# Kernel tuning notes

Hardware: AMD Instinct MI355X
Metric: run time of the kernel (lower is better)

## Reference

```python
import jax, jax.numpy as jnp
import numpy as np

EPS = 1e-05


def setup_inputs() -> dict:
    key = jax.random.key(0)
    ks = jax.random.split(key, 5)
    B, Q, M, DIM = 2, 1024, 1024, 3
    H, V, OUT, C = 8, 64, 512, 8
    # Chebyshev rational coefficients of exp(-x) (first C terms), expanded per head
    cheb_coeffs_expmx = np.array([
        0.4275836, -0.546424, 0.07106222, 0.05473271,
        0.005744192, -0.00792641, -0.005392865, -0.001210823,
    ], dtype=np.float32)
    cheb_coeffs = jnp.broadcast_to(jnp.asarray(cheb_coeffs_expmx)[None, :], (H, C))
    lengthscales = jnp.asarray([0.5, 1.0, 2.0, 4.0, 8.0, 16.0, 32.0, 64.0], dtype=jnp.float32)
    return {
        "query_positions": jax.random.normal(ks[0], (B, Q, DIM), dtype=jnp.float32),
        "key_positions": jax.random.normal(ks[1], (B, M, DIM), dtype=jnp.float32),
        "values": jax.random.normal(ks[2], (B, M, H, V), dtype=jnp.float32),
        "masked_elements": jnp.zeros((B, M), dtype=bool),
        "lengthscales": lengthscales,
        "cheb_coeffs": cheb_coeffs,
        "out_w": jax.random.normal(ks[3], (OUT, H * V), dtype=jnp.float32) * (1.0 / np.sqrt(H * V)),
    }


def _cheb_scores(x, coeffs):
    # x: [B,H,Q,M] squared scaled distances; coeffs: [H,C]
    # Chebyshev rational expansion: T0=1, T1=r, Tn = 2 r T_{n-1} - T_{n-2},
    # with r = (x-1)/(x+1). Accumulate sum_c coeffs[h,c] * T_c directly
    # instead of materializing the [B,H,C,Q,M] stack (same math).
    C = coeffs.shape[1]
    r = (x - 1.0) / (x + 1.0)
    tprev = jnp.ones_like(x)
    out = coeffs[None, :, 0, None, None] * tprev
    if C >= 2:
        tcur = r
        out = out + coeffs[None, :, 1, None, None] * tcur
        for c in range(2, C):
            tnext = 2.0 * r * tcur - tprev
            out = out + coeffs[None, :, c, None, None] * tnext
            tcur, tprev = tnext, tcur
    return out


def reference(query_positions, key_positions, values, masked_elements,
              lengthscales, cheb_coeffs, out_w):
    B, Q, _ = query_positions.shape
    H = lengthscales.shape[0]
    # force_asymptotic_zero: subtract per-head mean of coefficients
    coeffs = cheb_coeffs - jnp.mean(cheb_coeffs, axis=1, keepdims=True)
    # squared pairwise distances [B,Q,M] (cdist then squared == d2)
    d2 = jnp.sum((query_positions[:, :, None, :] - key_positions[:, None, :, :]) ** 2, axis=-1)
    # scaled squared distances per head: (d/ls)^2 -> [B,H,Q,M]
    x = d2[:, None, :, :] / (lengthscales[None, :, None, None] ** 2)
    scores = _cheb_scores(x, coeffs)
    # mask memory elements, then L1-normalise over memory axis
    scores = jnp.where(masked_elements[:, None, None, :], 0.0, scores)
    scores = scores / (jnp.sum(jnp.abs(scores), axis=-1, keepdims=True) + EPS)
    # attend: [B,H,Q,M] @ [B,H,M,V] -> [B,H,Q,V]
    attended = jnp.einsum('bhqm,bmhv->bhqv', scores, values)
    # flatten heads: [B,Q,H*V], then out projection (no bias)
    flat = attended.transpose(0, 2, 1, 3).reshape(B, Q, -1)
    return flat @ out_w.T
```

## Files before the change

### kernel.cpp

```cpp
#include <hip/hip_runtime.h>
#include <hip/hip_bf16.h>


typedef __attribute__((ext_vector_type(8))) short short8v;
typedef __attribute__((ext_vector_type(4))) short short4v;
typedef __attribute__((ext_vector_type(4))) float f32x4;

#define EPSF 1e-5f

__device__ __forceinline__ float frcp(float x) { return __builtin_amdgcn_rcpf(x); }
__device__ __forceinline__ short f2bf(float f) {
    __hip_bfloat16 h = __float2bfloat16(f);
    return *reinterpret_cast<short*>(&h);
}

#define VT_ELEMS   (2u * 8u * 64u * 1024u)
#define WB_OFF_S   (VT_ELEMS)
#define FLAT_OFF_S (VT_ELEMS + 512u * 512u)

__global__ __launch_bounds__(256) void prep(
    const float* __restrict__ vals, const float* __restrict__ outw,
    short* __restrict__ vt, short* __restrict__ wb)
{
    const int bid = blockIdx.x, t = threadIdx.x;
    if (bid < 256) {
        __shared__ float sf[64 * 68];
        const int b = bid >> 7, h = (bid >> 4) & 7, m0 = (bid & 15) * 64;
        #pragma unroll
        for (int fi = 0; fi < 4; ++fi) {
            const int idx = fi * 256 + t, mr = idx >> 4, c4 = idx & 15;
            const float4 v4 = *(const float4*)&vals[
                (((size_t)b * 1024 + m0 + mr) * 8 + h) * 64 + c4 * 4];
            *(float4*)&sf[mr * 68 + c4 * 4] = v4;
        }
        __syncthreads();
        const int v = t >> 2, mo = t & 3;
        short8v o0, o1;
        #pragma unroll
        for (int i = 0; i < 8; ++i) o0[i] = f2bf(sf[(mo * 16 + i) * 68 + v]);
        #pragma unroll
        for (int i = 0; i < 8; ++i) o1[i] = f2bf(sf[(mo * 16 + 8 + i) * 68 + v]);
        const size_t ob = ((size_t)(b * 8 + h) * 64 + v) * 1024 + m0 + mo * 16;
        *(short8v*)&vt[ob] = o0;
        *(short8v*)&vt[ob + 8] = o1;
    } else {
        const int wi = bid - 256;
        #pragma unroll
        for (int k = 0; k < 8; ++k) {
            const int fidx = wi * 8192 + k * 1024 + t * 4;
            const float4 f4 = *(const float4*)&outw[fidx];
            short4v s; s[0] = f2bf(f4.x); s[1] = f2bf(f4.y);
                       s[2] = f2bf(f4.z); s[3] = f2bf(f4.w);
            *(short4v*)&wb[fidx] = s;
        }
    }
}

__global__ __launch_bounds__(512, 4) void cheb_attn(
    const float* __restrict__ qp, const float* __restrict__ kp,
    const unsigned char* __restrict__ msk,
    const float* __restrict__ ls, const float* __restrict__ cheb,
    const short* __restrict__ vt, short* __restrict__ flatb)
{
    __shared__ float s_kx[1024], s_ky[1024], s_kz[1024];
    __shared__ __align__(8) unsigned char s_mask[1024];
    __shared__ float s_l1[4][32];
    __shared__ float s_pb[3][32 * 68];

    const int t = threadIdx.x;
    const int qt = blockIdx.x, h = blockIdx.y, b = blockIdx.z;
    const int w = t >> 6, lane = t & 63;
    const int wg = w & 1, g = w >> 1;
    const int arow = lane & 15, koct = lane >> 4;

    #pragma unroll
    for (int mm_ = 0; mm_ < 2; ++mm_) {
        const int m = mm_ * 512 + t;
        const size_t base = ((size_t)b * 1024 + m) * 3;
        s_kx[m] = kp[base + 0];
        s_ky[m] = kp[base + 1];
        s_kz[m] = kp[base + 2];
    }
    *(unsigned short*)&s_mask[t * 2] =
        *(const unsigned short*)&msk[(size_t)b * 1024 + t * 2];

    const float lsv = ls[h];
    const float invls2 = 1.0f / (lsv * lsv);
    float cc[8]; float cs = 0.f;
    #pragma unroll
    for (int j = 0; j < 8; ++j) { cc[j] = cheb[h * 8 + j]; cs += cc[j]; }
    const float cm = cs * 0.125f;
    #pragma unroll
    for (int j = 0; j < 8; ++j) cc[j] -= cm;

    const int qg = qt * 32 + wg * 16 + arow;
    const float qx = qp[((size_t)b * 1024 + qg) * 3 + 0];
    const float qy = qp[((size_t)b * 1024 + qg) * 3 + 1];
    const float qz = qp[((size_t)b * 1024 + qg) * 3 + 2];

    f32x4 acc[4] = {(f32x4)(0.f), (f32x4)(0.f), (f32x4)(0.f), (f32x4)(0.f)};
    const short* vtb = vt + ((size_t)(b * 8 + h) * 64) * 1024;
    float l1p = 0.f;

    __syncthreads();

    #pragma unroll
    for (int tile = 0; tile < 4; ++tile) {
        const int m0 = g * 256 + tile * 64;

        short8v bfr[2][4];
        #pragma unroll
        for (int kk = 0; kk < 2; ++kk)
            #pragma unroll
            for (int f = 0; f < 4; ++f)
                bfr[kk][f] = *(const short8v*)
                    &vtb[(size_t)(f * 16 + arow) * 1024 + m0 + kk * 32 + koct * 8];

        f32x4 kx[2][2], ky[2][2], kz[2][2];
        uint2 mmv[2];
        #pragma unroll
        for (int kk = 0; kk < 2; ++kk) {
            const int mb = m0 + kk * 32 + koct * 8;
            kx[kk][0] = *(const f32x4*)&s_kx[mb]; kx[kk][1] = *(const f32x4*)&s_kx[mb + 4];
            ky[kk][0] = *(const f32x4*)&s_ky[mb]; ky[kk][1] = *(const f32x4*)&s_ky[mb + 4];
            kz[kk][0] = *(const f32x4*)&s_kz[mb]; kz[kk][1] = *(const f32x4*)&s_kz[mb + 4];
            mmv[kk] = *(const uint2*)&s_mask[mb];
        }

        short8v a[2];
        #pragma unroll
        for (int kk = 0; kk < 2; ++kk) {
            const bool anymask = (mmv[kk].x | mmv[kk].y) != 0u;
            #pragma unroll
            for (int j = 0; j < 8; ++j) {
                const float dx = qx - kx[kk][j >> 2][j & 3];
                const float dy = qy - ky[kk][j >> 2][j & 3];
                const float dz = qz - kz[kk][j >> 2][j & 3];
                const float x  = (dx * dx + dy * dy + dz * dz) * invls2;
                const float r  = (x - 1.f) * frcp(x + 1.f);
                const float r2 = r + r;
                float tp = 1.f, tc = r;
                float s  = cc[0] + cc[1] * r;
                #pragma unroll
                for (int c = 2; c < 8; ++c) {
                    const float tn = r2 * tc - tp;
                    s += cc[c] * tn; tp = tc; tc = tn;
                }
                if (anymask) {
                    const unsigned int mword = (j < 4) ? mmv[kk].x : mmv[kk].y;
                    if ((mword >> ((j & 3) * 8)) & 0xffu) s = 0.f;
                }
                l1p += fabsf(s);
                a[kk][j] = f2bf(s);
            }
        }

        #pragma unroll
        for (int kk = 0; kk < 2; ++kk)
            #pragma unroll
            for (int f = 0; f < 4; ++f)
                acc[f] = __builtin_amdgcn_mfma_f32_16x16x32_bf16(
                    a[kk], bfr[kk][f], acc[f], 0, 0, 0);
    }

    l1p += __shfl_xor(l1p, 16);
    l1p += __shfl_xor(l1p, 32);
    if (koct == 0) s_l1[g][wg * 16 + arow] = l1p;

    if (g > 0) {
        #pragma unroll
        for (int f = 0; f < 4; ++f)
            #pragma unroll
            for (int j = 0; j < 4; ++j)
                s_pb[g - 1][(wg * 16 + koct * 4 + j) * 68 + f * 16 + arow] = acc[f][j];
    }
    __syncthreads();
    if (g == 0) {
        float rden[4];
        #pragma unroll
        for (int j = 0; j < 4; ++j) {
            const int row = wg * 16 + koct * 4 + j;
            rden[j] = frcp(s_l1[0][row] + s_l1[1][row] + s_l1[2][row]
                         + s_l1[3][row] + EPSF);
        }
        #pragma unroll
        for (int f = 0; f < 4; ++f)
            #pragma unroll
            for (int j = 0; j < 4; ++j) {
                const int row = wg * 16 + koct * 4 + j;
                const int col = f * 16 + arow;
                const float v = (acc[f][j]
                    + s_pb[0][row * 68 + col]
                    + s_pb[1][row * 68 + col]
                    + s_pb[2][row * 68 + col]) * rden[j];
                flatb[((size_t)b * 1024 + qt * 32 + row) * 512 + h * 64 + col]
                    = f2bf(v);
            }
    }
}

__global__ __launch_bounds__(256, 4) void proj(
    const short* __restrict__ flatb, const short* __restrict__ wb,
    float* __restrict__ out)
{
    const int t = threadIdx.x;
    const int r0 = blockIdx.x * 64, n0 = blockIdx.y * 32;
    const int w = t >> 6, lane = t & 63;
    const int arow = lane & 15, koct = lane >> 4;
    const int band = w * 16;

    f32x4 acc[2] = {(f32x4)(0.f), (f32x4)(0.f)};
    const short* ap = &flatb[(size_t)(r0 + band + arow) * 512];
    const short* b0 = &wb[(size_t)(n0 + arow) * 512];
    const short* b1 = &wb[(size_t)(n0 + 16 + arow) * 512];

    #pragma unroll 8
    for (int kk = 0; kk < 16; ++kk) {
        const int ko = kk * 32 + koct * 8;
        const short8v a   = *(const short8v*)&ap[ko];
        const short8v bf0 = *(const short8v*)&b0[ko];
        const short8v bf1 = *(const short8v*)&b1[ko];
        acc[0] = __builtin_amdgcn_mfma_f32_16x16x32_bf16(a, bf0, acc[0], 0, 0, 0);
        acc[1] = __builtin_amdgcn_mfma_f32_16x16x32_bf16(a, bf1, acc[1], 0, 0, 0);
    }
    #pragma unroll
    for (int f = 0; f < 2; ++f)
        #pragma unroll
        for (int j = 0; j < 4; ++j)
            out[((size_t)(r0 + band + koct * 4 + j)) * 512 + n0 + f * 16 + arow]
                = acc[f][j];
}

extern "C" void kernel_launch(void* const* d_in, const int* in_sizes, int n_in,
                              void* d_out, int out_size, void* d_ws, size_t ws_size,
                              hipStream_t stream) {
    const float* qp   = (const float*)d_in[0];
    const float* kp   = (const float*)d_in[1];
    const float* vals = (const float*)d_in[2];
    const unsigned char* msk = (const unsigned char*)d_in[3];
    const float* ls   = (const float*)d_in[4];
    const float* cheb = (const float*)d_in[5];
    const float* outw = (const float*)d_in[6];
    float* out = (float*)d_out;

    short* vtp   = (short*)d_ws;
    short* wbp   = vtp + WB_OFF_S;
    short* flatb = vtp + FLAT_OFF_S;

    prep<<<288, 256, 0, stream>>>(vals, outw, vtp, wbp);
    cheb_attn<<<dim3(32, 8, 2), 512, 0, stream>>>(qp, kp, msk, ls, cheb, vtp, flatb);
    proj<<<dim3(32, 16), 256, 0, stream>>>(flatb, wbp, out);
}
```

Baseline: 40.81 us.

## Fuse output projection into attention kernel via last-block atomic counter

Removes the separate projection kernel launch. Each attention block bumps a per-(batch, query-tile) counter after writing its head slice. The block that arrives last for that tile then computes the full 32x512 output projection from the bf16 flat buffer and bf16 weights. This saves one launch and its gap, but the projection work is serialized onto 64 last-arriving blocks, and those blocks read weights directly from global memory without reuse in shared memory.

```diff
diff --git a/kernel.cpp b/kernel.cpp
--- a/kernel.cpp
+++ b/kernel.cpp
@@ -17,10 +17,11 @@
 #define VT_ELEMS   (2u * 8u * 64u * 1024u)
 #define WB_OFF_S   (VT_ELEMS)
 #define FLAT_OFF_S (VT_ELEMS + 512u * 512u)
+#define CNT_OFF_S  (FLAT_OFF_S + 2u * 1024u * 512u)
 
 __global__ __launch_bounds__(256) void prep(
     const float* __restrict__ vals, const float* __restrict__ outw,
-    short* __restrict__ vt, short* __restrict__ wb)
+    short* __restrict__ vt, short* __restrict__ wb, int* __restrict__ cnt)
 {
     const int bid = blockIdx.x, t = threadIdx.x;
     if (bid < 256) {
@@ -45,6 +46,7 @@
         *(short8v*)&vt[ob + 8] = o1;
     } else {
         const int wi = bid - 256;
+        if (wi == 0 && t < 64) cnt[t] = 0;
         #pragma unroll
         for (int k = 0; k < 8; ++k) {
             const int fidx = wi * 8192 + k * 1024 + t * 4;
@@ -60,12 +62,15 @@
     const float* __restrict__ qp, const float* __restrict__ kp,
     const unsigned char* __restrict__ msk,
     const float* __restrict__ ls, const float* __restrict__ cheb,
-    const short* __restrict__ vt, short* __restrict__ flatb)
+    const short* __restrict__ vt, short* __restrict__ flatb,
+    const short* __restrict__ wb, float* __restrict__ out,
+    int* __restrict__ cnt)
 {
     __shared__ float s_kx[1024], s_ky[1024], s_kz[1024];
     __shared__ __align__(8) unsigned char s_mask[1024];
     __shared__ float s_l1[4][32];
     __shared__ float s_pb[3][32 * 68];
+    __shared__ int s_last;
 
     const int t = threadIdx.x;
     const int qt = blockIdx.x, h = blockIdx.y, b = blockIdx.z;
@@ -197,38 +202,45 @@
                     = f2bf(v);
             }
     }
-}
-
-__global__ __launch_bounds__(256, 4) void proj(
-    const short* __restrict__ flatb, const short* __restrict__ wb,
-    float* __restrict__ out)
-{
-    const int t = threadIdx.x;
-    const int r0 = blockIdx.x * 64, n0 = blockIdx.y * 32;
-    const int w = t >> 6, lane = t & 63;
-    const int arow = lane & 15, koct = lane >> 4;
-    const int band = w * 16;
-
-    f32x4 acc[2] = {(f32x4)(0.f), (f32x4)(0.f)};
-    const short* ap = &flatb[(size_t)(r0 + band + arow) * 512];
-    const short* b0 = &wb[(size_t)(n0 + arow) * 512];
-    const short* b1 = &wb[(size_t)(n0 + 16 + arow) * 512];
-
-    #pragma unroll 8
-    for (int kk = 0; kk < 16; ++kk) {
-        const int ko = kk * 32 + koct * 8;
-        const short8v a   = *(const short8v*)&ap[ko];
-        const short8v bf0 = *(const short8v*)&b0[ko];
-        const short8v bf1 = *(const short8v*)&b1[ko];
-        acc[0] = __builtin_amdgcn_mfma_f32_16x16x32_bf16(a, bf0, acc[0], 0, 0, 0);
-        acc[1] = __builtin_amdgcn_mfma_f32_16x16x32_bf16(a, bf1, acc[1], 0, 0, 0);
-    }
-    #pragma unroll
-    for (int f = 0; f < 2; ++f)
+
+    __syncthreads();
+    if (t == 0) {
+        __threadfence();
+        const int grp = b * 32 + qt;
+        const int prev = __hip_atomic_fetch_add(&cnt[grp], 1,
+                             __ATOMIC_RELEASE, __HIP_MEMORY_SCOPE_AGENT);
+        int last = 0;
+        if (prev == 7) {
+            (void)__hip_atomic_load(&cnt[grp], __ATOMIC_ACQUIRE,
+                                    __HIP_MEMORY_SCOPE_AGENT);
+            last = 1;
+        }
+        s_last = last;
+    }
+    __syncthreads();
+    if (!s_last) return;
+
+    const int rb = w & 1, ng = w >> 1;
+    f32x4 pacc[8] = {(f32x4)(0.f), (f32x4)(0.f), (f32x4)(0.f), (f32x4)(0.f),
+                     (f32x4)(0.f), (f32x4)(0.f), (f32x4)(0.f), (f32x4)(0.f)};
+    const short* ap = &flatb[((size_t)b * 1024 + qt * 32 + rb * 16 + arow) * 512];
+    #pragma unroll 4
+    for (int kk2 = 0; kk2 < 16; ++kk2) {
+        const int ko = kk2 * 32 + koct * 8;
+        const short8v af = *(const short8v*)&ap[ko];
+        #pragma unroll
+        for (int nt = 0; nt < 8; ++nt) {
+            const short8v bf = *(const short8v*)
+                &wb[(size_t)(ng * 128 + nt * 16 + arow) * 512 + ko];
+            pacc[nt] = __builtin_amdgcn_mfma_f32_16x16x32_bf16(af, bf, pacc[nt], 0, 0, 0);
+        }
+    }
+    #pragma unroll
+    for (int nt = 0; nt < 8; ++nt)
         #pragma unroll
         for (int j = 0; j < 4; ++j)
-            out[((size_t)(r0 + band + koct * 4 + j)) * 512 + n0 + f * 16 + arow]
-                = acc[f][j];
+            out[((size_t)b * 1024 + qt * 32 + rb * 16 + koct * 4 + j) * 512
+                + ng * 128 + nt * 16 + arow] = pacc[nt][j];
 }
 
 extern "C" void kernel_launch(void* const* d_in, const int* in_sizes, int n_in,
@@ -246,8 +258,9 @@
     short* vtp   = (short*)d_ws;
     short* wbp   = vtp + WB_OFF_S;
     short* flatb = vtp + FLAT_OFF_S;
-
-    prep<<<288, 256, 0, stream>>>(vals, outw, vtp, wbp);
-    cheb_attn<<<dim3(32, 8, 2), 512, 0, stream>>>(qp, kp, msk, ls, cheb, vtp, flatb);
-    proj<<<dim3(32, 16), 256, 0, stream>>>(flatb, wbp, out);
-}
+    int*   cnt   = (int*)(vtp + CNT_OFF_S);
+
+    prep<<<288, 256, 0, stream>>>(vals, outw, vtp, wbp, cnt);
+    cheb_attn<<<dim3(32, 8, 2), 512, 0, stream>>>(qp, kp, msk, ls, cheb,
+                                                  vtp, flatb, wbp, out, cnt);
+}
```

After: 113.3 us. +177.7%, slower.

## Split attention into 16-query blocks with 8-way key split and aliased LDS

Applied to the files above, without the earlier changes.

Each cheb_attn block now handles 16 queries instead of 32, and all 8 waves split the key dimension (128 keys each), so the grid doubles to 1024 blocks. The key/mask staging buffers and the partial-sum reduction buffer now alias one shared allocation, behind an added barrier, to keep LDS per block small, and launch bounds ask for 8 blocks per CU. The final reduction is spread across all threads. The aim is more parallelism and occupancy, at the cost of recomputing key staging per block, twice the V-tile reads from global memory, and an 8-way reduction through LDS.

```diff
diff --git a/kernel.cpp b/kernel.cpp
--- a/kernel.cpp
+++ b/kernel.cpp
@@ -56,21 +56,25 @@
     }
 }
 
-__global__ __launch_bounds__(512, 4) void cheb_attn(
+#define LDS_BYTES 35328
+__global__ __launch_bounds__(512, 8) void cheb_attn(
     const float* __restrict__ qp, const float* __restrict__ kp,
     const unsigned char* __restrict__ msk,
     const float* __restrict__ ls, const float* __restrict__ cheb,
     const short* __restrict__ vt, short* __restrict__ flatb)
 {
-    __shared__ float s_kx[1024], s_ky[1024], s_kz[1024];
-    __shared__ __align__(8) unsigned char s_mask[1024];
-    __shared__ float s_l1[4][32];
-    __shared__ float s_pb[3][32 * 68];
+    __shared__ __align__(16) unsigned char smem[LDS_BYTES];
+    float* s_kx = (float*)smem;
+    float* s_ky = s_kx + 1024;
+    float* s_kz = s_ky + 1024;
+    unsigned char* s_mask = (unsigned char*)(s_kz + 1024);
+    float* s_pb = (float*)smem;
+    float* s_l1 = s_pb + 8 * 16 * 68;
 
     const int t = threadIdx.x;
     const int qt = blockIdx.x, h = blockIdx.y, b = blockIdx.z;
     const int w = t >> 6, lane = t & 63;
-    const int wg = w & 1, g = w >> 1;
+    const int g = w;
     const int arow = lane & 15, koct = lane >> 4;
 
     #pragma unroll
@@ -93,7 +97,7 @@
     #pragma unroll
     for (int j = 0; j < 8; ++j) cc[j] -= cm;
 
-    const int qg = qt * 32 + wg * 16 + arow;
+    const int qg = qt * 16 + arow;
     const float qx = qp[((size_t)b * 1024 + qg) * 3 + 0];
     const float qy = qp[((size_t)b * 1024 + qg) * 3 + 1];
     const float qz = qp[((size_t)b * 1024 + qg) * 3 + 2];
@@ -105,8 +109,8 @@
     __syncthreads();
 
     #pragma unroll
-    for (int tile = 0; tile < 4; ++tile) {
-        const int m0 = g * 256 + tile * 64;
+    for (int tile = 0; tile < 2; ++tile) {
+        const int m0 = g * 128 + tile * 64;
 
         short8v bfr[2][4];
         #pragma unroll
@@ -165,37 +169,30 @@
 
     l1p += __shfl_xor(l1p, 16);
     l1p += __shfl_xor(l1p, 32);
-    if (koct == 0) s_l1[g][wg * 16 + arow] = l1p;
-
-    if (g > 0) {
-        #pragma unroll
-        for (int f = 0; f < 4; ++f)
-            #pragma unroll
-            for (int j = 0; j < 4; ++j)
-                s_pb[g - 1][(wg * 16 + koct * 4 + j) * 68 + f * 16 + arow] = acc[f][j];
-    }
+
     __syncthreads();
-    if (g == 0) {
-        float rden[4];
-        #pragma unroll
-        for (int j = 0; j < 4; ++j) {
-            const int row = wg * 16 + koct * 4 + j;
-            rden[j] = frcp(s_l1[0][row] + s_l1[1][row] + s_l1[2][row]
-                         + s_l1[3][row] + EPSF);
-        }
-        #pragma unroll
-        for (int f = 0; f < 4; ++f)
-            #pragma unroll
-            for (int j = 0; j < 4; ++j) {
-                const int row = wg * 16 + koct * 4 + j;
-                const int col = f * 16 + arow;
-                const float v = (acc[f][j]
-                    + s_pb[0][row * 68 + col]
-                    + s_pb[1][row * 68 + col]
-                    + s_pb[2][row * 68 + col]) * rden[j];
-                flatb[((size_t)b * 1024 + qt * 32 + row) * 512 + h * 64 + col]
-                    = f2bf(v);
-            }
+
+    if (koct == 0) s_l1[g * 16 + arow] = l1p;
+    #pragma unroll
+    for (int f = 0; f < 4; ++f)
+        #pragma unroll
+        for (int j = 0; j < 4; ++j)
+            s_pb[(g * 16 * 68) + (koct * 4 + j) * 68 + f * 16 + arow] = acc[f][j];
+    __syncthreads();
+
+    #pragma unroll
+    for (int v = 0; v < 2; ++v) {
+        const int vid = v * 512 + t;
+        const int row = vid >> 6, col = vid & 63;
+        float den = s_l1[row];
+        #pragma unroll
+        for (int gg = 1; gg < 8; ++gg) den += s_l1[gg * 16 + row];
+        const float rden = frcp(den + EPSF);
+        float sum = s_pb[row * 68 + col];
+        #pragma unroll
+        for (int gg = 1; gg < 8; ++gg) sum += s_pb[gg * 16 * 68 + row * 68 + col];
+        flatb[((size_t)b * 1024 + qt * 16 + row) * 512 + h * 64 + col]
+            = f2bf(sum * rden);
     }
 }
 
@@ -248,6 +245,6 @@
     short* flatb = vtp + FLAT_OFF_S;
 
     prep<<<288, 256, 0, stream>>>(vals, outw, vtp, wbp);
-    cheb_attn<<<dim3(32, 8, 2), 512, 0, stream>>>(qp, kp, msk, ls, cheb, vtp, flatb);
+    cheb_attn<<<dim3(64, 8, 2), 512, 0, stream>>>(qp, kp, msk, ls, cheb, vtp, flatb);
     proj<<<dim3(32, 16), 256, 0, stream>>>(flatb, wbp, out);
 }
```

Measured after the change: 58.28 us. 42.8% more time.

## Drop prep kernel; convert values and out_w to bf16 inline at use

Applied to the files above, without the earlier changes.

Removes the separate prep kernel that transposed values to bf16 and converted out_w to bf16. The attention kernel now gathers fp32 values directly with strided scalar loads and converts them per MFMA fragment, and the projection kernel loads fp32 weights and converts them inline. This saves one kernel launch and a round trip of the workspace writes, at the cost of uncoalesced 4-byte gathers (stride 512 floats) and redundant conversion work in the attention inner loop.

```diff
diff --git a/kernel.cpp b/kernel.cpp
--- a/kernel.cpp
+++ b/kernel.cpp
@@ -3,7 +3,6 @@
 
 
 typedef __attribute__((ext_vector_type(8))) short short8v;
-typedef __attribute__((ext_vector_type(4))) short short4v;
 typedef __attribute__((ext_vector_type(4))) float f32x4;
 
 #define EPSF 1e-5f
@@ -14,53 +13,11 @@
     return *reinterpret_cast<short*>(&h);
 }
 
-#define VT_ELEMS   (2u * 8u * 64u * 1024u)
-#define WB_OFF_S   (VT_ELEMS)
-#define FLAT_OFF_S (VT_ELEMS + 512u * 512u)
-
-__global__ __launch_bounds__(256) void prep(
-    const float* __restrict__ vals, const float* __restrict__ outw,
-    short* __restrict__ vt, short* __restrict__ wb)
-{
-    const int bid = blockIdx.x, t = threadIdx.x;
-    if (bid < 256) {
-        __shared__ float sf[64 * 68];
-        const int b = bid >> 7, h = (bid >> 4) & 7, m0 = (bid & 15) * 64;
-        #pragma unroll
-        for (int fi = 0; fi < 4; ++fi) {
-            const int idx = fi * 256 + t, mr = idx >> 4, c4 = idx & 15;
-            const float4 v4 = *(const float4*)&vals[
-                (((size_t)b * 1024 + m0 + mr) * 8 + h) * 64 + c4 * 4];
-            *(float4*)&sf[mr * 68 + c4 * 4] = v4;
-        }
-        __syncthreads();
-        const int v = t >> 2, mo = t & 3;
-        short8v o0, o1;
-        #pragma unroll
-        for (int i = 0; i < 8; ++i) o0[i] = f2bf(sf[(mo * 16 + i) * 68 + v]);
-        #pragma unroll
-        for (int i = 0; i < 8; ++i) o1[i] = f2bf(sf[(mo * 16 + 8 + i) * 68 + v]);
-        const size_t ob = ((size_t)(b * 8 + h) * 64 + v) * 1024 + m0 + mo * 16;
-        *(short8v*)&vt[ob] = o0;
-        *(short8v*)&vt[ob + 8] = o1;
-    } else {
-        const int wi = bid - 256;
-        #pragma unroll
-        for (int k = 0; k < 8; ++k) {
-            const int fidx = wi * 8192 + k * 1024 + t * 4;
-            const float4 f4 = *(const float4*)&outw[fidx];
-            short4v s; s[0] = f2bf(f4.x); s[1] = f2bf(f4.y);
-                       s[2] = f2bf(f4.z); s[3] = f2bf(f4.w);
-            *(short4v*)&wb[fidx] = s;
-        }
-    }
-}
-
 __global__ __launch_bounds__(512, 4) void cheb_attn(
     const float* __restrict__ qp, const float* __restrict__ kp,
     const unsigned char* __restrict__ msk,
     const float* __restrict__ ls, const float* __restrict__ cheb,
-    const short* __restrict__ vt, short* __restrict__ flatb)
+    const float* __restrict__ vals, short* __restrict__ flatb)
 {
     __shared__ float s_kx[1024], s_ky[1024], s_kz[1024];
     __shared__ __align__(8) unsigned char s_mask[1024];
@@ -99,7 +56,7 @@
     const float qz = qp[((size_t)b * 1024 + qg) * 3 + 2];
 
     f32x4 acc[4] = {(f32x4)(0.f), (f32x4)(0.f), (f32x4)(0.f), (f32x4)(0.f)};
-    const short* vtb = vt + ((size_t)(b * 8 + h) * 64) * 1024;
+    const float* vpl = vals + (size_t)b * 1024 * 512 + h * 64;
     float l1p = 0.f;
 
     __syncthreads();
@@ -107,14 +64,6 @@
     #pragma unroll
     for (int tile = 0; tile < 4; ++tile) {
         const int m0 = g * 256 + tile * 64;
-
-        short8v bfr[2][4];
-        #pragma unroll
-        for (int kk = 0; kk < 2; ++kk)
-            #pragma unroll
-            for (int f = 0; f < 4; ++f)
-                bfr[kk][f] = *(const short8v*)
-                    &vtb[(size_t)(f * 16 + arow) * 1024 + m0 + kk * 32 + koct * 8];
 
         f32x4 kx[2][2], ky[2][2], kz[2][2];
         uint2 mmv[2];
@@ -156,11 +105,18 @@
         }
 
         #pragma unroll
-        for (int kk = 0; kk < 2; ++kk)
-            #pragma unroll
-            for (int f = 0; f < 4; ++f)
+        for (int kk = 0; kk < 2; ++kk) {
+            const float* vb = vpl + (size_t)(m0 + kk * 32 + koct * 8) * 512 + arow;
+            #pragma unroll
+            for (int f = 0; f < 4; ++f) {
+                short8v bfv;
+                #pragma unroll
+                for (int j = 0; j < 8; ++j)
+                    bfv[j] = f2bf(vb[j * 512 + f * 16]);
                 acc[f] = __builtin_amdgcn_mfma_f32_16x16x32_bf16(
-                    a[kk], bfr[kk][f], acc[f], 0, 0, 0);
+                    a[kk], bfv, acc[f], 0, 0, 0);
+            }
+        }
     }
 
     l1p += __shfl_xor(l1p, 16);
@@ -200,7 +156,7 @@
 }
 
 __global__ __launch_bounds__(256, 4) void proj(
-    const short* __restrict__ flatb, const short* __restrict__ wb,
+    const short* __restrict__ flatb, const float* __restrict__ outw,
     float* __restrict__ out)
 {
     const int t = threadIdx.x;
@@ -211,15 +167,22 @@
 
     f32x4 acc[2] = {(f32x4)(0.f), (f32x4)(0.f)};
     const short* ap = &flatb[(size_t)(r0 + band + arow) * 512];
-    const short* b0 = &wb[(size_t)(n0 + arow) * 512];
-    const short* b1 = &wb[(size_t)(n0 + 16 + arow) * 512];
+    const float* w0 = &outw[(size_t)(n0 + arow) * 512];
+    const float* w1 = &outw[(size_t)(n0 + 16 + arow) * 512];
 
     #pragma unroll 8
     for (int kk = 0; kk < 16; ++kk) {
         const int ko = kk * 32 + koct * 8;
-        const short8v a   = *(const short8v*)&ap[ko];
-        const short8v bf0 = *(const short8v*)&b0[ko];
-        const short8v bf1 = *(const short8v*)&b1[ko];
+        const short8v a = *(const short8v*)&ap[ko];
+        const float4 wa0 = *(const float4*)&w0[ko];
+        const float4 wb0 = *(const float4*)&w0[ko + 4];
+        const float4 wa1 = *(const float4*)&w1[ko];
+        const float4 wb1 = *(const float4*)&w1[ko + 4];
+        short8v bf0, bf1;
+        bf0[0] = f2bf(wa0.x); bf0[1] = f2bf(wa0.y); bf0[2] = f2bf(wa0.z); bf0[3] = f2bf(wa0.w);
+        bf0[4] = f2bf(wb0.x); bf0[5] = f2bf(wb0.y); bf0[6] = f2bf(wb0.z); bf0[7] = f2bf(wb0.w);
+        bf1[0] = f2bf(wa1.x); bf1[1] = f2bf(wa1.y); bf1[2] = f2bf(wa1.z); bf1[3] = f2bf(wa1.w);
+        bf1[4] = f2bf(wb1.x); bf1[5] = f2bf(wb1.y); bf1[6] = f2bf(wb1.z); bf1[7] = f2bf(wb1.w);
         acc[0] = __builtin_amdgcn_mfma_f32_16x16x32_bf16(a, bf0, acc[0], 0, 0, 0);
         acc[1] = __builtin_amdgcn_mfma_f32_16x16x32_bf16(a, bf1, acc[1], 0, 0, 0);
     }
@@ -243,11 +206,8 @@
     const float* outw = (const float*)d_in[6];
     float* out = (float*)d_out;
 
-    short* vtp   = (short*)d_ws;
-    short* wbp   = vtp + WB_OFF_S;
-    short* flatb = vtp + FLAT_OFF_S;
-
-    prep<<<288, 256, 0, stream>>>(vals, outw, vtp, wbp);
-    cheb_attn<<<dim3(32, 8, 2), 512, 0, stream>>>(qp, kp, msk, ls, cheb, vtp, flatb);
-    proj<<<dim3(32, 16), 256, 0, stream>>>(flatb, wbp, out);
-}
+    short* flatb = (short*)d_ws;
+
+    cheb_attn<<<dim3(32, 8, 2), 512, 0, stream>>>(qp, kp, msk, ls, cheb, vals, flatb);
+    proj<<<dim3(32, 16), 256, 0, stream>>>(flatb, outw, out);
+}
```

After: 44.29 us. 8.5% more time.
